# Optimization experiments

Measured on AMD Instinct MI355X. Metric: run time of the kernel, lower is better.

## Reference

```python
import jax, jax.numpy as jnp
import numpy as np

EPS = 1e-8  # torch F.cosine_similarity norm clamp


def setup_inputs() -> dict:
    key = jax.random.key(0)
    k1, k2, k3, k4 = jax.random.split(key, 4)
    B, N, M, D, T = 8, 4096, 2048, 512, 2
    return {
        "features": jax.random.normal(k1, (B, N, D), dtype=jnp.float32),
        "text": jax.random.normal(k2, (T, M, D), dtype=jnp.float32),
        "W": jax.random.normal(k3, (D, D), dtype=jnp.float32) * 0.02,
        "b": jax.random.normal(k4, (D,), dtype=jnp.float32) * 0.02,
    }


def reference(features, text, W, b):
    # features: [B, N, D] (output of the extractor), text: [T, M, D]
    B, N, D = features.shape
    f1 = jnp.einsum("bnd,de->bne", features, W) + b  # linear_layer(features)
    t1 = text[1]  # [M, D]; expanded across batch (row 1 per original code)

    # cosine similarity over last dim without materializing [B, N, M, D]
    fn = f1 / jnp.maximum(jnp.linalg.norm(f1, axis=-1, keepdims=True), EPS)
    tn = t1 / jnp.maximum(jnp.linalg.norm(t1, axis=-1, keepdims=True), EPS)
    sim = jnp.einsum("bnd,md->bnm", fn, tn)  # [B, N, M]

    e = jnp.exp(sim)
    w = e / jnp.sum(e, axis=1, keepdims=True)  # normalize over N (dim=1)

    # features_t [B,D,N] @ w [B,N,M] -> [B,D,M] -> transpose -> [B,M,D]
    fm = jnp.einsum("bnd,bnm->bmd", features, w)

    t1b = jnp.broadcast_to(t1[None, :, :], (B,) + t1.shape)  # [B, M, D]
    combine_feature = jnp.concatenate([fm, t1b], axis=2)  # [B, M, 2D]
    return combine_feature
```

## Files before the change

kernel.cpp:

```cpp
#include <hip/hip_runtime.h>

#define B_SZ 8
#define N_SZ 4096
#define M_SZ 2048
#define D_SZ 512

typedef __attribute__((ext_vector_type(8))) short bf16x8;
typedef __attribute__((ext_vector_type(4))) float f32x4;
typedef __attribute__((address_space(1))) const void* gptr1;
typedef __attribute__((address_space(3))) void* lptr3;

__device__ __forceinline__ unsigned short f2bf(float x) {
    unsigned int u = __builtin_bit_cast(unsigned int, x);
    u += 0x7fffu + ((u >> 16) & 1u);
    return (unsigned short)(u >> 16);
}
__device__ __forceinline__ float bf2f(unsigned short u) {
    unsigned int x = ((unsigned int)u) << 16;
    return __builtin_bit_cast(float, x);
}

__device__ __forceinline__ void vmcnt0() { asm volatile("s_waitcnt vmcnt(0)" ::: "memory"); }
__device__ __forceinline__ void vmcnt3() { asm volatile("s_waitcnt vmcnt(3)" ::: "memory"); }
__device__ __forceinline__ void vmcnt4() { asm volatile("s_waitcnt vmcnt(4)" ::: "memory"); }
template<int BN> __device__ __forceinline__ void vmcnt_steady() {
    if constexpr (BN == 256) vmcnt4(); else vmcnt3();
}

template<int NROWS>
__device__ __forceinline__ void stage_half(
    const unsigned short* __restrict__ G, int ld, int grow0, int k0,
    unsigned short* lds, int tid)
{
    const int w = tid >> 6, l = tid & 63;
#pragma unroll
    for (int c = 0; c < NROWS / 64; ++c) {
        const int idx  = (c * 8 + w) * 64 + l;
        const int row  = idx >> 3;
        const int slot = (idx & 7) ^ (row & 7);
        const unsigned short* ga = G + (size_t)(grow0 + row) * ld + (k0 + slot * 8);
        __builtin_amdgcn_global_load_lds((gptr1)ga, (lptr3)(lds + (c * 8 + w) * 512), 16, 0, 0);
    }
}

#define PH_RA(BUF, QM)                                                                \
    _Pragma("unroll") for (int mi = 0; mi < 4; ++mi)                                  \
      _Pragma("unroll") for (int ks = 0; ks < 2; ++ks) {                              \
        const int row = (QM) * 128 + wrow + mi * 16 + lr;                             \
        af[mi][ks] = *(const bf16x8*)(As + (BUF) * ABUF + row * 64 + (((ks * 4 + kq) ^ (row & 7)) * 8)); \
      }

#define PH_RB(BUF, QN, DST)                                                           \
    _Pragma("unroll") for (int ni = 0; ni < NF2; ++ni)                                \
      _Pragma("unroll") for (int ks = 0; ks < 2; ++ks) {                              \
        const int row = (QN) * (BN / 2) + wcol + ni * 16 + lr;                        \
        DST[ni][ks] = *(const bf16x8*)(Bs + (BUF) * BBUF + row * 64 + (((ks * 4 + kq) ^ (row & 7)) * 8)); \
      }

#define PH_MMA(QM, QN, BQ, STAGES, TAIL)                                              \
  {                                                                                   \
    STAGES;                                                                           \
    __builtin_amdgcn_s_barrier();                                                     \
    __builtin_amdgcn_s_setprio(1);                                                    \
    _Pragma("unroll") for (int mi = 0; mi < 4; ++mi)                                  \
      _Pragma("unroll") for (int ni = 0; ni < NF2; ++ni)                              \
        _Pragma("unroll") for (int ks = 0; ks < 2; ++ks)                              \
          acc[(QM) * 4 + mi][(QN) * NF2 + ni] = __builtin_amdgcn_mfma_f32_16x16x32_bf16( \
              af[mi][ks], BQ[ni][ks], acc[(QM) * 4 + mi][(QN) * NF2 + ni], 0, 0, 0);  \
    __builtin_amdgcn_s_setprio(0);                                                    \
    TAIL;                                                                             \
    __builtin_amdgcn_s_barrier();                                                     \
  }

template<int BN>
__device__ __forceinline__ void mainloop8(
    const unsigned short* __restrict__ A, const unsigned short* __restrict__ Bt,
    int lda, int ldb, int rowBase, int colBase, int K,
    unsigned short* As, unsigned short* Bs, f32x4 (&acc)[8][BN / 64])
{
    constexpr int NF2  = BN / 128;
    constexpr int BNH  = BN / 2;
    constexpr int ABUF = 256 * 64, AH = 128 * 64;
    constexpr int BBUF = BN * 64,  BH = BNH * 64;
    const int tid = threadIdx.x, lane = tid & 63, w = tid >> 6;
    const int wrow = (w >> 2) * 64;
    const int wcol = (w & 3) * (BN / 8);
    const int lr = lane & 15, kq = lane >> 4;
    const int niter = K >> 7;

    bf16x8 af[4][2], bq0[NF2][2], bq1[NF2][2];

    stage_half<128>(A,  lda, rowBase,       0,  As,        tid);
    stage_half<BNH>(Bt, ldb, colBase,       0,  Bs,        tid);
    stage_half<128>(A,  lda, rowBase + 128, 0,  As + AH,   tid);
    stage_half<BNH>(Bt, ldb, colBase + BNH, 0,  Bs + BH,   tid);
    stage_half<128>(A,  lda, rowBase,       64, As + ABUF, tid);
    stage_half<BNH>(Bt, ldb, colBase,       64, Bs + BBUF, tid);
    vmcnt_steady<BN>();
    __builtin_amdgcn_s_barrier();

    for (int I = 0; I < niter; ++I) {
        const bool nl = (I + 1 < niter);
        const int ke = I << 7;
        PH_RA(0, 0) PH_RB(0, 0, bq0)
        PH_MMA(0, 0, bq0, { stage_half<128>(A,  lda, rowBase + 128, ke + 64,  As + ABUF + AH, tid); }, {})
        PH_RB(0, 1, bq1)
        PH_MMA(0, 1, bq1, { stage_half<BNH>(Bt, ldb, colBase + BNH, ke + 64,  Bs + BBUF + BH, tid); }, {})
        PH_RA(0, 1)
        PH_MMA(1, 1, bq1, { if (nl) stage_half<128>(A,  lda, rowBase,       ke + 128, As,      tid); }, {})
        PH_MMA(1, 0, bq0, { if (nl) stage_half<BNH>(Bt, ldb, colBase,       ke + 128, Bs,      tid); },
                          { if (nl) vmcnt_steady<BN>(); else vmcnt0(); })
        PH_RA(1, 0) PH_RB(1, 0, bq0)
        PH_MMA(0, 0, bq0, { if (nl) stage_half<128>(A,  lda, rowBase + 128, ke + 128, As + AH, tid); }, {})
        PH_RB(1, 1, bq1)
        PH_MMA(0, 1, bq1, { if (nl) stage_half<BNH>(Bt, ldb, colBase + BNH, ke + 128, Bs + BH, tid); }, {})
        PH_RA(1, 1)
        PH_MMA(1, 1, bq1, { if (nl) stage_half<128>(A,  lda, rowBase,       ke + 192, As + ABUF, tid); }, {})
        PH_MMA(1, 0, bq0, { if (nl) stage_half<BNH>(Bt, ldb, colBase,       ke + 192, Bs + BBUF, tid); },
                          { if (nl) vmcnt_steady<BN>(); })
    }
}

__global__ __launch_bounds__(256) void prep_tn_k(
    const float* __restrict__ text, unsigned short* __restrict__ tn,
    float* __restrict__ out, float* __restrict__ L, float* __restrict__ SS)
{
    const int m = blockIdx.x;
    const int t = threadIdx.x;
    const float* t1 = text + (size_t)M_SZ * D_SZ;
    float2 v = ((const float2*)(t1 + (size_t)m * D_SZ))[t];
    float s = v.x * v.x + v.y * v.y;
#pragma unroll
    for (int off = 32; off > 0; off >>= 1) s += __shfl_down(s, off);
    __shared__ float partial[4];
    if ((t & 63) == 0) partial[t >> 6] = s;
    __syncthreads();
    float norm = sqrtf(partial[0] + partial[1] + partial[2] + partial[3]);
    norm = fmaxf(norm, 1e-8f);
    const float inv = 1.f / norm;
    ushort2 pk; pk.x = f2bf(v.x * inv); pk.y = f2bf(v.y * inv);
    ((ushort2*)(tn + (size_t)m * D_SZ))[t] = pk;
#pragma unroll
    for (int b = 0; b < B_SZ; ++b)
        ((float2*)(out + ((size_t)(b * M_SZ + m)) * (2 * D_SZ) + D_SZ))[t] = v;
    if (m < 64) L[m * 256 + t] = 0.f;
    if (m < 128) SS[m * 256 + t] = 0.f;
}

__global__ __launch_bounds__(256) void prep_w_k(
    const float* __restrict__ W, unsigned short* __restrict__ Wt)
{
    const int dt = blockIdx.x, et = blockIdx.y;
    const int t = threadIdx.x;
    __shared__ unsigned short tile[64][72];
    const int rr = t >> 4;
    const int cc = (t & 15) * 4;
#pragma unroll
    for (int p = 0; p < 4; ++p) {
        const int d = p * 16 + rr;
        const float4 v = *(const float4*)(W + (size_t)(dt * 64 + d) * D_SZ + et * 64 + cc);
        tile[d][cc] = f2bf(v.x); tile[d][cc + 1] = f2bf(v.y);
        tile[d][cc + 2] = f2bf(v.z); tile[d][cc + 3] = f2bf(v.w);
    }
    __syncthreads();
#pragma unroll
    for (int p = 0; p < 4; ++p) {
        const int e = p * 16 + rr;
        ushort4 pk;
        pk.x = tile[cc][e]; pk.y = tile[cc + 1][e]; pk.z = tile[cc + 2][e]; pk.w = tile[cc + 3][e];
        *(ushort4*)(Wt + (size_t)(et * 64 + e) * D_SZ + dt * 64 + cc) = pk;
    }
}

__global__ __launch_bounds__(256) void convert_feat_k(
    const float* __restrict__ feat, unsigned short* __restrict__ V,
    unsigned short* __restrict__ Vt)
{
    const int nt = blockIdx.x, dt = blockIdx.y, b = blockIdx.z;
    const int t = threadIdx.x;
    __shared__ unsigned short tile[64][72];
    const int rr = t >> 4;
    const int cc = (t & 15) * 4;
#pragma unroll
    for (int p = 0; p < 4; ++p) {
        const int r = p * 16 + rr;
        const size_t grow = (size_t)(b * N_SZ + nt * 64 + r);
        const float4 v = *(const float4*)(feat + grow * D_SZ + dt * 64 + cc);
        ushort4 pk; pk.x = f2bf(v.x); pk.y = f2bf(v.y); pk.z = f2bf(v.z); pk.w = f2bf(v.w);
        *(ushort4*)(V + grow * D_SZ + dt * 64 + cc) = pk;
        tile[r][cc] = pk.x; tile[r][cc + 1] = pk.y; tile[r][cc + 2] = pk.z; tile[r][cc + 3] = pk.w;
    }
    __syncthreads();
#pragma unroll
    for (int p = 0; p < 4; ++p) {
        const int d = p * 16 + rr;
        ushort4 pk;
        pk.x = tile[cc][d]; pk.y = tile[cc + 1][d]; pk.z = tile[cc + 2][d]; pk.w = tile[cc + 3][d];
        *(ushort4*)(Vt + ((size_t)(b * D_SZ + dt * 64 + d)) * N_SZ + nt * 64 + cc) = pk;
    }
}

__global__ __launch_bounds__(512, 1) void gemm1_k8(
    const unsigned short* __restrict__ V, const unsigned short* __restrict__ Wt,
    const float* __restrict__ bias, unsigned short* __restrict__ f1b,
    float* __restrict__ SS)
{
    __shared__ unsigned short smem[65536];
    unsigned short* As = smem;
    unsigned short* Bs = smem + 32768;
    f32x4 acc[8][4];
#pragma unroll
    for (int i = 0; i < 8; ++i)
#pragma unroll
        for (int j = 0; j < 4; ++j) acc[i][j] = (f32x4){0.f, 0.f, 0.f, 0.f};

    const int lin = blockIdx.x;
    const int rowBase = (lin >> 1) * 256;
    const int colBase = (lin & 1) * 256;

    mainloop8<256>(V, Wt, D_SZ, D_SZ, rowBase, colBase, D_SZ, As, Bs, acc);

    const int tid = threadIdx.x, lane = tid & 63, w = tid >> 6;
    const int wrow = (w >> 2) * 64, wcol = (w & 3) * 32;
    const int lr = lane & 15, kq = lane >> 4;

    float bv[4];
    int cs[4];
#pragma unroll
    for (int j = 0; j < 4; ++j) {
        cs[j] = colBase + (j >> 1) * 128 + wcol + (j & 1) * 16 + lr;
        bv[j] = bias[cs[j]];
    }
#pragma unroll
    for (int a = 0; a < 8; ++a) {
        const int r0 = rowBase + (a >> 2) * 128 + wrow + (a & 3) * 16 + kq * 4;
        float s[4] = {0.f, 0.f, 0.f, 0.f};
#pragma unroll
        for (int j = 0; j < 4; ++j) {
#pragma unroll
            for (int r = 0; r < 4; ++r) {
                const float v = acc[a][j][r] + bv[j];
                f1b[(size_t)(r0 + r) * D_SZ + cs[j]] = f2bf(v);
                s[r] += v * v;
            }
        }
#pragma unroll
        for (int off = 1; off <= 8; off <<= 1)
#pragma unroll
            for (int r = 0; r < 4; ++r) s[r] += __shfl_xor(s[r], off);
        if (lr == 0) {
#pragma unroll
            for (int r = 0; r < 4; ++r) atomicAdd(&SS[r0 + r], s[r]);
        }
    }
}

__global__ __launch_bounds__(512, 1) void gemm2_k8(
    const unsigned short* __restrict__ f1b, const unsigned short* __restrict__ tn,
    const float* __restrict__ SS, unsigned short* __restrict__ E,
    float* __restrict__ L)
{
    __shared__ unsigned short smem[65536];
    __shared__ float invn[256];
    unsigned short* As = smem;
    unsigned short* Bs = smem + 32768;
    f32x4 acc[8][4];
#pragma unroll
    for (int i = 0; i < 8; ++i)
#pragma unroll
        for (int j = 0; j < 4; ++j) acc[i][j] = (f32x4){0.f, 0.f, 0.f, 0.f};

    const int lin = blockIdx.x;
    const int xcd = lin & 7, slot = lin >> 3;
    const int mt = slot & 7;
    const int rt = (slot >> 3) * 8 + xcd;
    const int rowBase = rt * 256;
    const int colBase = mt * 256;

    mainloop8<256>(f1b, tn, D_SZ, D_SZ, rowBase, colBase, D_SZ, As, Bs, acc);

    const int tid = threadIdx.x, lane = tid & 63, w = tid >> 6;
    if (tid < 256) {
        const float ss = SS[rowBase + tid];
        invn[tid] = 1.f / fmaxf(sqrtf(ss), 1e-8f);
    }
    __syncthreads();

    const int wrow = (w >> 2) * 64, wcol = (w & 3) * 32;
    const int lr = lane & 15, kq = lane >> 4;
    const int b = rowBase >> 12;
    const int nb0 = rowBase & 4095;

    unsigned short* P = smem;
    float ps[4] = {0.f, 0.f, 0.f, 0.f};
#pragma unroll
    for (int a = 0; a < 8; ++a) {
        const int n0 = (a >> 2) * 128 + wrow + (a & 3) * 16 + kq * 4;
        const float4 inr = *(const float4*)(invn + n0);
#pragma unroll
        for (int j = 0; j < 4; ++j) {
            const int m = (j >> 1) * 128 + wcol + (j & 1) * 16 + lr;
            const float e0 = __expf(acc[a][j][0] * inr.x);
            const float e1 = __expf(acc[a][j][1] * inr.y);
            const float e2 = __expf(acc[a][j][2] * inr.z);
            const float e3 = __expf(acc[a][j][3] * inr.w);
            ushort4 pk; pk.x = f2bf(e0); pk.y = f2bf(e1); pk.z = f2bf(e2); pk.w = f2bf(e3);
            *(ushort4*)(P + m * 256 + (((n0 >> 3) ^ (m & 7)) * 8) + (n0 & 7)) = pk;
            ps[j] += (e0 + e1) + (e2 + e3);
        }
    }
#pragma unroll
    for (int j = 0; j < 4; ++j) {
        float p = ps[j];
        p += __shfl_down(p, 16);
        p += __shfl_down(p, 32);
        const int m = (j >> 1) * 128 + wcol + (j & 1) * 16 + lr;
        if (lane < 16) atomicAdd(&L[b * M_SZ + colBase + m], p);
    }
    __syncthreads();

    unsigned short* Eb = E + (size_t)b * M_SZ * N_SZ;
#pragma unroll
    for (int c = 0; c < 16; ++c) {
        const int rm = c * 16 + (tid >> 5);
        const int ns = tid & 31;
        bf16x8 v = *(const bf16x8*)(P + rm * 256 + ((ns ^ (rm & 7)) * 8));
        *(bf16x8*)(Eb + (size_t)(colBase + rm) * N_SZ + nb0 + ns * 8) = v;
    }
}

__global__ __launch_bounds__(512, 1) void gemm3_k8(
    const unsigned short* __restrict__ E, const unsigned short* __restrict__ Vt,
    const float* __restrict__ L, float* __restrict__ out)
{
    __shared__ unsigned short smem[49152];
    unsigned short* As = smem;
    unsigned short* Bs = smem + 32768;
    f32x4 acc[8][2];
#pragma unroll
    for (int i = 0; i < 8; ++i)
#pragma unroll
        for (int j = 0; j < 2; ++j) acc[i][j] = (f32x4){0.f, 0.f, 0.f, 0.f};

    const int lin = blockIdx.x;
    const int b = lin & 7;
    const int mtile = (lin >> 3) & 7;
    const int dt = lin >> 6;
    const int rowBase = mtile * 256;
    const int colBase = dt * 128;

    const unsigned short* Ab = E + (size_t)b * M_SZ * N_SZ;
    const unsigned short* Bb = Vt + (size_t)b * D_SZ * N_SZ;
    mainloop8<128>(Ab, Bb, N_SZ, N_SZ, rowBase, colBase, N_SZ, As, Bs, acc);

    const int tid = threadIdx.x, lane = tid & 63, w = tid >> 6;
    const int wrow = (w >> 2) * 64, wcol = (w & 3) * 16;
    const int lr = lane & 15, kq = lane >> 4;

#pragma unroll
    for (int a = 0; a < 8; ++a) {
        const int r0 = rowBase + (a >> 2) * 128 + wrow + (a & 3) * 16 + kq * 4;
        float invl[4];
#pragma unroll
        for (int r = 0; r < 4; ++r) invl[r] = 1.f / L[b * M_SZ + r0 + r];
#pragma unroll
        for (int j = 0; j < 2; ++j) {
            const int d = colBase + j * 64 + wcol + lr;
#pragma unroll
            for (int r = 0; r < 4; ++r)
                out[((size_t)(b * M_SZ + r0 + r)) * (2 * D_SZ) + d] = acc[a][j][r] * invl[r];
        }
    }
}

extern "C" void kernel_launch(void* const* d_in, const int* in_sizes, int n_in,
                              void* d_out, int out_size, void* d_ws, size_t ws_size,
                              hipStream_t stream) {
    const float* features = (const float*)d_in[0];
    const float* text     = (const float*)d_in[1];
    const float* W        = (const float*)d_in[2];
    const float* bias     = (const float*)d_in[3];
    float* out = (float*)d_out;
    char* ws = (char*)d_ws;

    unsigned short* f1b = (unsigned short*)(ws + 0);
    unsigned short* tn  = (unsigned short*)(ws + 33554432);
    unsigned short* Wt  = (unsigned short*)(ws + 35651584);
    unsigned short* V   = (unsigned short*)(ws + 36175872);
    unsigned short* Vt  = (unsigned short*)(ws + 69730304);
    float*          L   = (float*)(ws + 103284736);
    float*          SS  = (float*)(ws + 103350272);
    unsigned short* E   = (unsigned short*)(ws + 103481344);

    hipLaunchKernelGGL(prep_tn_k, dim3(M_SZ), dim3(256), 0, stream, text, tn, out, L, SS);
    hipLaunchKernelGGL(prep_w_k, dim3(8, 8), dim3(256), 0, stream, W, Wt);
    hipLaunchKernelGGL(convert_feat_k, dim3(64, 8, 8), dim3(256), 0, stream, features, V, Vt);
    hipLaunchKernelGGL(gemm1_k8, dim3(256), dim3(512), 0, stream, V, Wt, bias, f1b, SS);
    hipLaunchKernelGGL(gemm2_k8, dim3(1024), dim3(512), 0, stream, f1b, tn, SS, E, L);
    hipLaunchKernelGGL(gemm3_k8, dim3(256), dim3(512), 0, stream, E, Vt, L, out);
}
```

Before: 354.1 us.

## Deepen prefetch schedule in third GEMM mainloop with earlier global loads

Adds a DEEP variant of the shared mainloop that preloads the second B half before the loop and issues each stage's next-tile loads one MMA phase earlier. The vmcnt waits are loosened to match, so more global-to-LDS loads stay in flight. It is enabled only for the K=4096 weighted-sum GEMM, to hide memory latency over its long K loop. The risk is LDS buffer reuse hazards if a buffer is overwritten before all waves have read it, and the reordering may bring little gain.

```diff
diff --git a/kernel.cpp b/kernel.cpp
--- a/kernel.cpp
+++ b/kernel.cpp
@@ -23,8 +23,10 @@
 __device__ __forceinline__ void vmcnt0() { asm volatile("s_waitcnt vmcnt(0)" ::: "memory"); }
 __device__ __forceinline__ void vmcnt3() { asm volatile("s_waitcnt vmcnt(3)" ::: "memory"); }
 __device__ __forceinline__ void vmcnt4() { asm volatile("s_waitcnt vmcnt(4)" ::: "memory"); }
-template<int BN> __device__ __forceinline__ void vmcnt_steady() {
-    if constexpr (BN == 256) vmcnt4(); else vmcnt3();
+__device__ __forceinline__ void vmcnt6() { asm volatile("s_waitcnt vmcnt(6)" ::: "memory"); }
+template<int BN, bool DEEP> __device__ __forceinline__ void vmcnt_steady() {
+    if constexpr (DEEP) { if constexpr (BN == 256) vmcnt6(); else vmcnt4(); }
+    else               { if constexpr (BN == 256) vmcnt4(); else vmcnt3(); }
 }
 
 template<int NROWS>
@@ -72,7 +74,7 @@
     __builtin_amdgcn_s_barrier();                                                     \
   }
 
-template<int BN>
+template<int BN, bool DEEP>
 __device__ __forceinline__ void mainloop8(
     const unsigned short* __restrict__ A, const unsigned short* __restrict__ Bt,
     int lda, int ldb, int rowBase, int colBase, int K,
@@ -88,6 +90,8 @@
     const int lr = lane & 15, kq = lane >> 4;
     const int niter = K >> 7;
 
+    auto certify = [&]() { vmcnt_steady<BN, DEEP>(); };
+
     bf16x8 af[4][2], bq0[NF2][2], bq1[NF2][2];
 
     stage_half<128>(A,  lda, rowBase,       0,  As,        tid);
@@ -96,7 +100,8 @@
     stage_half<BNH>(Bt, ldb, colBase + BNH, 0,  Bs + BH,   tid);
     stage_half<128>(A,  lda, rowBase,       64, As + ABUF, tid);
     stage_half<BNH>(Bt, ldb, colBase,       64, Bs + BBUF, tid);
-    vmcnt_steady<BN>();
+    if constexpr (DEEP) stage_half<BNH>(Bt, ldb, colBase + BNH, 64, Bs + BBUF + BH, tid);
+    certify();
     __builtin_amdgcn_s_barrier();
 
     for (int I = 0; I < niter; ++I) {
@@ -105,19 +110,31 @@
         PH_RA(0, 0) PH_RB(0, 0, bq0)
         PH_MMA(0, 0, bq0, { stage_half<128>(A,  lda, rowBase + 128, ke + 64,  As + ABUF + AH, tid); }, {})
         PH_RB(0, 1, bq1)
-        PH_MMA(0, 1, bq1, { stage_half<BNH>(Bt, ldb, colBase + BNH, ke + 64,  Bs + BBUF + BH, tid); }, {})
+        PH_MMA(0, 1, bq1,
+            { if constexpr (DEEP) { if (nl) stage_half<128>(A,  lda, rowBase,       ke + 128, As,      tid); }
+              else                {          stage_half<BNH>(Bt, ldb, colBase + BNH, ke + 64,  Bs + BBUF + BH, tid); } }, {})
         PH_RA(0, 1)
-        PH_MMA(1, 1, bq1, { if (nl) stage_half<128>(A,  lda, rowBase,       ke + 128, As,      tid); }, {})
-        PH_MMA(1, 0, bq0, { if (nl) stage_half<BNH>(Bt, ldb, colBase,       ke + 128, Bs,      tid); },
-                          { if (nl) vmcnt_steady<BN>(); else vmcnt0(); })
+        PH_MMA(1, 1, bq1,
+            { if constexpr (DEEP) { if (nl) stage_half<BNH>(Bt, ldb, colBase,       ke + 128, Bs,      tid); }
+              else                { if (nl) stage_half<128>(A,  lda, rowBase,       ke + 128, As,      tid); } }, {})
+        PH_MMA(1, 0, bq0,
+            { if constexpr (DEEP) { if (nl) stage_half<BNH>(Bt, ldb, colBase + BNH, ke + 128, Bs + BH, tid); }
+              else                { if (nl) stage_half<BNH>(Bt, ldb, colBase,       ke + 128, Bs,      tid); } },
+            { if (nl) certify(); else vmcnt0(); })
         PH_RA(1, 0) PH_RB(1, 0, bq0)
         PH_MMA(0, 0, bq0, { if (nl) stage_half<128>(A,  lda, rowBase + 128, ke + 128, As + AH, tid); }, {})
         PH_RB(1, 1, bq1)
-        PH_MMA(0, 1, bq1, { if (nl) stage_half<BNH>(Bt, ldb, colBase + BNH, ke + 128, Bs + BH, tid); }, {})
+        PH_MMA(0, 1, bq1,
+            { if constexpr (DEEP) { if (nl) stage_half<128>(A,  lda, rowBase,       ke + 192, As + ABUF, tid); }
+              else                { if (nl) stage_half<BNH>(Bt, ldb, colBase + BNH, ke + 128, Bs + BH,   tid); } }, {})
         PH_RA(1, 1)
-        PH_MMA(1, 1, bq1, { if (nl) stage_half<128>(A,  lda, rowBase,       ke + 192, As + ABUF, tid); }, {})
-        PH_MMA(1, 0, bq0, { if (nl) stage_half<BNH>(Bt, ldb, colBase,       ke + 192, Bs + BBUF, tid); },
-                          { if (nl) vmcnt_steady<BN>(); })
+        PH_MMA(1, 1, bq1,
+            { if constexpr (DEEP) { if (nl) stage_half<BNH>(Bt, ldb, colBase,       ke + 192, Bs + BBUF, tid); }
+              else                { if (nl) stage_half<128>(A,  lda, rowBase,       ke + 192, As + ABUF, tid); } }, {})
+        PH_MMA(1, 0, bq0,
+            { if constexpr (DEEP) { if (nl) stage_half<BNH>(Bt, ldb, colBase + BNH, ke + 192, Bs + BBUF + BH, tid); }
+              else                { if (nl) stage_half<BNH>(Bt, ldb, colBase,       ke + 192, Bs + BBUF,      tid); } },
+            { if (nl) certify(); })
     }
 }
 
@@ -218,7 +235,7 @@
     const int rowBase = (lin >> 1) * 256;
     const int colBase = (lin & 1) * 256;
 
-    mainloop8<256>(V, Wt, D_SZ, D_SZ, rowBase, colBase, D_SZ, As, Bs, acc);
+    mainloop8<256, false>(V, Wt, D_SZ, D_SZ, rowBase, colBase, D_SZ, As, Bs, acc);
 
     const int tid = threadIdx.x, lane = tid & 63, w = tid >> 6;
     const int wrow = (w >> 2) * 64, wcol = (w & 3) * 32;
@@ -277,7 +294,7 @@
     const int rowBase = rt * 256;
     const int colBase = mt * 256;
 
-    mainloop8<256>(f1b, tn, D_SZ, D_SZ, rowBase, colBase, D_SZ, As, Bs, acc);
+    mainloop8<256, false>(f1b, tn, D_SZ, D_SZ, rowBase, colBase, D_SZ, As, Bs, acc);
 
     const int tid = threadIdx.x, lane = tid & 63, w = tid >> 6;
     if (tid < 256) {
@@ -351,7 +368,7 @@
 
     const unsigned short* Ab = E + (size_t)b * M_SZ * N_SZ;
     const unsigned short* Bb = Vt + (size_t)b * D_SZ * N_SZ;
-    mainloop8<128>(Ab, Bb, N_SZ, N_SZ, rowBase, colBase, N_SZ, As, Bs, acc);
+    mainloop8<128, true>(Ab, Bb, N_SZ, N_SZ, rowBase, colBase, N_SZ, As, Bs, acc);
 
     const int tid = threadIdx.x, lane = tid & 63, w = tid >> 6;
     const int wrow = (w >> 2) * 64, wcol = (w & 3) * 16;
```

Measured after the change: 355.8 us. About the same (+0.5%).
